# Kernel tuning notes

Hardware: AMD Instinct MI355X
Metric: run time of the kernel (lower is better)

Reference implementation:

```python
import jax, jax.numpy as jnp
import numpy as np

K = 1024  # codebook size
D = 256   # embedding dim


def setup_inputs() -> dict:
    key = jax.random.key(0)
    k1, k2 = jax.random.split(key)
    z_e_x = jax.random.normal(k1, (32, D, 32, 32), dtype=jnp.float32)  # NCHW
    # nn.Embedding weight initialized uniform(-1/K, 1/K)
    W = jax.random.uniform(k2, (K, D), dtype=jnp.float32, minval=-1.0 / K, maxval=1.0 / K)
    return {"z_e_x": z_e_x, "W": W}


def reference(z_e_x, W):
    # permute NCHW -> NHWC, flatten spatial, nearest-codebook lookup (vq)
    z = jnp.transpose(z_e_x, (0, 2, 3, 1))            # [B, H, Wd, D]
    B, H, Wd, Dd = z.shape
    flat = z.reshape(-1, Dd)                           # [N, D]
    # squared L2 distances: ||z||^2 - 2 z.W^T + ||W||^2
    z_sq = jnp.sum(flat * flat, axis=1, keepdims=True)         # [N, 1]
    w_sq = jnp.sum(W * W, axis=1)                               # [K]
    dists = z_sq - 2.0 * (flat @ W.T) + w_sq[None, :]           # [N, K]
    idx = jnp.argmin(dists, axis=1)                             # [N]
    latents = idx.reshape(B, H, Wd)                             # [B, H, Wd] int indices
    return latents
```

## Files before the change

kernel.cpp:

```cpp
#include <hip/hip_runtime.h>

#define NPOS 32768
#define DDIM 256
#define KCODES 1024

typedef __attribute__((ext_vector_type(8))) short bf16x8;
typedef __attribute__((ext_vector_type(4))) float f32x4;
typedef unsigned long long u64;

__device__ __forceinline__ float sqr_rn(float x) {
    float r = x * x;
    asm volatile("" : "+v"(r));
    return r;
}
__device__ __forceinline__ float add_rn(float a, float b) {
    float r = a + b;
    asm volatile("" : "+v"(r));
    return r;
}

__device__ __forceinline__ unsigned short f2bf(float x) {
    unsigned u = __float_as_uint(x);
    return (unsigned short)((u + 0x7fffu + ((u >> 16) & 1u)) >> 16);
}

__device__ __forceinline__ u64 packm(float s, int code) {
    unsigned b = __float_as_uint(s);
    unsigned mm = ((unsigned)((int)b >> 31)) | 0x80000000u;
    return ((u64)(b ^ mm) << 32) | (unsigned)code;
}

__device__ __forceinline__ void gld16(const void* g, void* lds) {
    __builtin_amdgcn_global_load_lds(
        (const __attribute__((address_space(1))) unsigned int*)g,
        (__attribute__((address_space(3))) unsigned int*)lds, 16, 0, 0);
}

__global__ __launch_bounds__(256) void zconv(const float* __restrict__ z,
                                             unsigned short* __restrict__ zb16t) {
    __shared__ unsigned short Ls[8 * 1024];
    const int t   = threadIdx.x;
    const int img = blockIdx.x >> 5;
    const int dc  = blockIdx.x & 31;
    const int kk  = dc >> 2, kq = dc & 3;
    const float* zr = z + img * (DDIM * 1024) + dc * 8 * 1024;
#pragma unroll
    for (int e = 0; e < 8; ++e) {
        const float4 v = *(const float4*)&zr[e * 1024 + t * 4];
        unsigned short* o = &Ls[e * 1024 + t * 4];
        o[0] = f2bf(v.x); o[1] = f2bf(v.y); o[2] = f2bf(v.z); o[3] = f2bf(v.w);
    }
    __syncthreads();
#pragma unroll
    for (int j = 0; j < 4; ++j) {
        const int m = t + j * 256;
        const int mtile = img * 8 + (m >> 7);
        bf16x8 o;
#pragma unroll
        for (int e = 0; e < 8; ++e) o[e] = (short)Ls[e * 1024 + m];
        *(bf16x8*)&zb16t[mtile * 32768 + kk * 4096 + kq * 1024 + (m & 127) * 8] = o;
    }
}

__global__ __launch_bounds__(256) void wprep(const float* __restrict__ W,
                                             float* __restrict__ wsq,
                                             unsigned short* __restrict__ wb16t) {
    const int t   = threadIdx.x;
    const int row = blockIdx.x * 16 + (t >> 4);
    const int j   = t & 15;
    const float* base = W + row * DDIM + (j & 7) + (j >> 3) * 128;
    float r = sqr_rn(base[0]);
#pragma unroll
    for (int i = 1; i < 16; ++i) r = add_rn(r, sqr_rn(base[i * 8]));
#pragma unroll
    for (int m = 1; m <= 8; m <<= 1) r = add_rn(r, __shfl_xor(r, m));
    if (j == 0) wsq[row] = r;

#pragma unroll
    for (int jj = 0; jj < 2; ++jj) {
        const int u  = t + jj * 256;
        const int n  = blockIdx.x * 16 + (u >> 5);
        const int k8 = u & 31;
        const float4 f0 = *(const float4*)&W[n * DDIM + k8 * 8];
        const float4 f1 = *(const float4*)&W[n * DDIM + k8 * 8 + 4];
        bf16x8 o;
        o[0] = (short)f2bf(f0.x); o[1] = (short)f2bf(f0.y);
        o[2] = (short)f2bf(f0.z); o[3] = (short)f2bf(f0.w);
        o[4] = (short)f2bf(f1.x); o[5] = (short)f2bf(f1.y);
        o[6] = (short)f2bf(f1.z); o[7] = (short)f2bf(f1.w);
        const int kk = k8 >> 2, kq = k8 & 3;
        *(bf16x8*)&wb16t[(n >> 8) * 65536 + kk * 8192 + kq * 2048 + (n & 255) * 8] = o;
    }
}

__global__ __launch_bounds__(256) __attribute__((amdgpu_waves_per_eu(2, 2)))
void gemm_top2(const unsigned short* __restrict__ zb16t,
               const unsigned short* __restrict__ wb16t,
               const float* __restrict__ wsq, u64* __restrict__ cand) {
    __shared__ u64 redU[4096];
    char* Ab = (char*)redU;
    char* Bb = (char*)redU + 8192;

    const int t    = threadIdx.x;
    const int w    = t >> 6;
    const int l    = t & 63;
    const int lg   = l * 16;
    const int ln   = l & 15;
    const int q    = l >> 4;
    const int mw   = (w & 1) * 64;
    const int nw   = (w >> 1) * 128;
    const int mblk = blockIdx.x >> 2;
    const int nblk = blockIdx.x & 3;
    const int m0   = mblk * 128;
    const int n0   = nblk * 256;

    const char* Az = (const char*)zb16t + (size_t)mblk * 65536;
    const char* Bz = (const char*)wb16t + (size_t)nblk * 131072;

    f32x4 acc[4][8];
#pragma unroll
    for (int a = 0; a < 4; ++a)
#pragma unroll
        for (int b = 0; b < 8; ++b) acc[a][b] = (f32x4)(0.f);

#pragma unroll 1
    for (int kk = 0; kk < 8; ++kk) {
        const char* a = Az + kk * 8192 + lg;
        const char* b = Bz + kk * 16384 + lg;
        gld16(a + w * 1024,        Ab + w * 1024);
        gld16(a + (4 + w) * 1024,  Ab + (4 + w) * 1024);
        gld16(b + w * 1024,        Bb + w * 1024);
        gld16(b + (4 + w) * 1024,  Bb + (4 + w) * 1024);
        gld16(b + (8 + w) * 1024,  Bb + (8 + w) * 1024);
        gld16(b + (12 + w) * 1024, Bb + (12 + w) * 1024);
        __syncthreads();
        bf16x8 afr[4];
#pragma unroll
        for (int mf = 0; mf < 4; ++mf)
            afr[mf] = *(const bf16x8*)(Ab + q * 2048 + (mw + mf * 16 + ln) * 16);
#pragma unroll
        for (int nf = 0; nf < 8; ++nf) {
            const bf16x8 bfr = *(const bf16x8*)(Bb + q * 4096 + (nw + nf * 16 + ln) * 16);
#pragma unroll
            for (int mf = 0; mf < 4; ++mf)
                acc[mf][nf] = __builtin_amdgcn_mfma_f32_16x16x32_bf16(
                    afr[mf], bfr, acc[mf][nf], 0, 0, 0);
        }
        __syncthreads();
    }

    float wq[8];
#pragma unroll
    for (int nf = 0; nf < 8; ++nf) wq[nf] = wsq[n0 + nw + nf * 16 + ln];

#pragma unroll
    for (int mf = 0; mf < 4; ++mf) {
#pragma unroll
        for (int reg = 0; reg < 4; ++reg) {
            const int row = mw + mf * 16 + q * 4 + reg;
            float s0 = 1e30f, s1 = 1e30f;
            int   i0 = 0,     i1 = 0;
#pragma unroll
            for (int nf = 0; nf < 8; ++nf) {
                const float s  = fmaf(-2.f, acc[mf][nf][reg], wq[nf]);
                const int   cc = n0 + nw + nf * 16 + ln;
                if (s < s0)      { s1 = s0; i1 = i0; s0 = s; i0 = cc; }
                else if (s < s1) { s1 = s; i1 = cc; }
            }
            u64 p0 = packm(s0, i0), p1 = packm(s1, i1);
            const u64 o0 = __shfl_xor(p0, 1);
            const u64 o1 = __shfl_xor(p1, 1);
            const u64 c0 = (p0 < o0) ? p0 : o0;
            const u64 hi = (p0 < o0) ? o0 : p0;
            const u64 lo = (p1 < o1) ? p1 : o1;
            const u64 c1 = (hi < lo) ? hi : lo;
            if ((ln & 1) == 0) {
                u64* slot = &redU[row * 32 + (w >> 1) * 16 + (ln >> 1) * 2];
                slot[0] = c0;
                slot[1] = c1;
            }
        }
    }
    __syncthreads();
    {
        const int r2 = t >> 1, half = t & 1;
        u64 c0 = ~0ull, c1 = ~0ull;
#pragma unroll
        for (int j = 0; j < 16; ++j) {
            const u64 v = redU[r2 * 32 + half * 16 + j];
            if (v < c0)      { c1 = c0; c0 = v; }
            else if (v < c1) { c1 = v; }
        }
        __syncthreads();
        redU[r2 * 4 + half * 2]     = c0;
        redU[r2 * 4 + half * 2 + 1] = c1;
    }
    __syncthreads();
    if (t < 128) {
        const u64 a = redU[t * 4], b = redU[t * 4 + 1];
        const u64 c = redU[t * 4 + 2], d = redU[t * 4 + 3];
        const u64 m1 = (a < c) ? a : c;
        const u64 hi = (a < c) ? c : a;
        const u64 lo = (b < d) ? b : d;
        const u64 m2 = (hi < lo) ? hi : lo;
        u64* o = &cand[(u64)(m0 + t) * 8 + nblk * 2];
        o[0] = m1;
        o[1] = m2;
    }
}

#define ZS 260
__global__ __launch_bounds__(256) void rescore(const float* __restrict__ z,
                                               const float* __restrict__ W,
                                               const float* __restrict__ wsq,
                                               const u64* __restrict__ cand,
                                               int* __restrict__ out) {
    __shared__ float Zs[32 * ZS];
    const int t  = threadIdx.x;
    const int m0 = blockIdx.x * 32;
    const float* zimg = z + (m0 >> 10) * (DDIM * 1024) + (m0 & 1023);
#pragma unroll
    for (int j = 0; j < 8; ++j) {
        const int f4 = t + j * 256;
        const int d = f4 >> 3, p4 = f4 & 7;
        const float4 v = *(const float4*)&zimg[d * 1024 + p4 * 4];
        Zs[(p4 * 4 + 0) * ZS + d] = v.x;
        Zs[(p4 * 4 + 1) * ZS + d] = v.y;
        Zs[(p4 * 4 + 2) * ZS + d] = v.z;
        Zs[(p4 * 4 + 3) * ZS + d] = v.w;
    }
    __syncthreads();
    const int pl = t >> 3, slot = t & 7;
    const int p = m0 + pl;
    const float* zr = &Zs[pl * ZS];

    float h0 = sqr_rn(zr[slot]);
    float h1 = sqr_rn(zr[128 + slot]);
#pragma unroll
    for (int i = 1; i < 16; ++i) {
        h0 = add_rn(h0, sqr_rn(zr[slot + 8 * i]));
        h1 = add_rn(h1, sqr_rn(zr[128 + slot + 8 * i]));
    }
#pragma unroll
    for (int m = 1; m <= 4; m <<= 1) {
        h0 = add_rn(h0, __shfl_xor(h0, m));
        h1 = add_rn(h1, __shfl_xor(h1, m));
    }
    const float zq = add_rn(h0, h1);

    const int code = (int)(unsigned)(cand[(u64)p * 8 + slot] & 0xffffffffULL);
    const float* wr = W + code * DDIM;
    float M = 0.f;
#pragma unroll 8
    for (int d4 = 0; d4 < 64; ++d4) {
        const float4 zv = *(const float4*)&zr[d4 * 4];
        const float4 wv = *(const float4*)&wr[d4 * 4];
        M = fmaf(zv.x, wv.x, M);
        M = fmaf(zv.y, wv.y, M);
        M = fmaf(zv.z, wv.z, M);
        M = fmaf(zv.w, wv.w, M);
    }
    const float s = add_rn(fmaf(-2.f, M, zq), wsq[code]);
    u64 v = ((u64)__float_as_uint(s) << 32) | (unsigned)code;
#pragma unroll
    for (int m = 1; m <= 4; m <<= 1) {
        const u64 o = __shfl_xor(v, m);
        if (o < v) v = o;
    }
    if (slot == 0) out[p] = (int)(unsigned)(v & 0xffffffffULL);
}

extern "C" void kernel_launch(void* const* d_in, const int* in_sizes, int n_in,
                              void* d_out, int out_size, void* d_ws, size_t ws_size,
                              hipStream_t stream) {
    const float* z = (const float*)d_in[0];
    const float* W = (const float*)d_in[1];
    int* out = (int*)d_out;

    char* ws = (char*)d_ws;
    float*          wsq   = (float*)ws;
    u64*            cand  = (u64*)(ws + 4096);
    unsigned short* zb16t = (unsigned short*)(ws + 2101248);
    unsigned short* wb16t = (unsigned short*)(ws + 18878464);

    wprep<<<KCODES / 16, 256, 0, stream>>>(W, wsq, wb16t);
    zconv<<<32 * 32, 256, 0, stream>>>(z, zb16t);
    gemm_top2<<<(NPOS / 128) * 4, 256, 0, stream>>>(zb16t, wb16t, wsq, cand);
    rescore<<<NPOS / 32, 256, 0, stream>>>(z, W, wsq, cand, out);
}
```

Baseline: 149.0 us.

## Merge prep kernels and load GEMM fragments directly from global memory

Combines the W and z conversion kernels into a single launch, using a block-index split, to save one kernel launch. The GEMM main loop stops staging A and B tiles through LDS with global_load_lds and barriers. Each lane now reads its bf16 MFMA fragments straight from the pre-swizzled global layout. This removes the LDS round trip and both syncthreads per k-step, at the cost of redundant global and L2 traffic across waves that share fragments, and less latency hiding.

```diff
diff --git a/kernel.cpp b/kernel.cpp
--- a/kernel.cpp
+++ b/kernel.cpp
@@ -30,66 +30,60 @@
     return ((u64)(b ^ mm) << 32) | (unsigned)code;
 }
 
-__device__ __forceinline__ void gld16(const void* g, void* lds) {
-    __builtin_amdgcn_global_load_lds(
-        (const __attribute__((address_space(1))) unsigned int*)g,
-        (__attribute__((address_space(3))) unsigned int*)lds, 16, 0, 0);
-}
-
-__global__ __launch_bounds__(256) void zconv(const float* __restrict__ z,
-                                             unsigned short* __restrict__ zb16t) {
+__global__ __launch_bounds__(256) void prep(const float* __restrict__ z,
+                                            const float* __restrict__ W,
+                                            float* __restrict__ wsq,
+                                            unsigned short* __restrict__ zb16t,
+                                            unsigned short* __restrict__ wb16t) {
     __shared__ unsigned short Ls[8 * 1024];
-    const int t   = threadIdx.x;
-    const int img = blockIdx.x >> 5;
-    const int dc  = blockIdx.x & 31;
-    const int kk  = dc >> 2, kq = dc & 3;
-    const float* zr = z + img * (DDIM * 1024) + dc * 8 * 1024;
-#pragma unroll
-    for (int e = 0; e < 8; ++e) {
-        const float4 v = *(const float4*)&zr[e * 1024 + t * 4];
-        unsigned short* o = &Ls[e * 1024 + t * 4];
-        o[0] = f2bf(v.x); o[1] = f2bf(v.y); o[2] = f2bf(v.z); o[3] = f2bf(v.w);
-    }
-    __syncthreads();
-#pragma unroll
-    for (int j = 0; j < 4; ++j) {
-        const int m = t + j * 256;
-        const int mtile = img * 8 + (m >> 7);
-        bf16x8 o;
-#pragma unroll
-        for (int e = 0; e < 8; ++e) o[e] = (short)Ls[e * 1024 + m];
-        *(bf16x8*)&zb16t[mtile * 32768 + kk * 4096 + kq * 1024 + (m & 127) * 8] = o;
-    }
-}
-
-__global__ __launch_bounds__(256) void wprep(const float* __restrict__ W,
-                                             float* __restrict__ wsq,
-                                             unsigned short* __restrict__ wb16t) {
-    const int t   = threadIdx.x;
-    const int row = blockIdx.x * 16 + (t >> 4);
-    const int j   = t & 15;
-    const float* base = W + row * DDIM + (j & 7) + (j >> 3) * 128;
-    float r = sqr_rn(base[0]);
-#pragma unroll
-    for (int i = 1; i < 16; ++i) r = add_rn(r, sqr_rn(base[i * 8]));
-#pragma unroll
-    for (int m = 1; m <= 8; m <<= 1) r = add_rn(r, __shfl_xor(r, m));
-    if (j == 0) wsq[row] = r;
-
-#pragma unroll
-    for (int jj = 0; jj < 2; ++jj) {
-        const int u  = t + jj * 256;
-        const int n  = blockIdx.x * 16 + (u >> 5);
-        const int k8 = u & 31;
-        const float4 f0 = *(const float4*)&W[n * DDIM + k8 * 8];
-        const float4 f1 = *(const float4*)&W[n * DDIM + k8 * 8 + 4];
-        bf16x8 o;
-        o[0] = (short)f2bf(f0.x); o[1] = (short)f2bf(f0.y);
-        o[2] = (short)f2bf(f0.z); o[3] = (short)f2bf(f0.w);
-        o[4] = (short)f2bf(f1.x); o[5] = (short)f2bf(f1.y);
-        o[6] = (short)f2bf(f1.z); o[7] = (short)f2bf(f1.w);
-        const int kk = k8 >> 2, kq = k8 & 3;
-        *(bf16x8*)&wb16t[(n >> 8) * 65536 + kk * 8192 + kq * 2048 + (n & 255) * 8] = o;
+    const int t = threadIdx.x;
+    if (blockIdx.x < 1024) {
+        const int img = blockIdx.x >> 5;
+        const int dc  = blockIdx.x & 31;
+        const int kk  = dc >> 2, kq = dc & 3;
+        const float* zr = z + img * (DDIM * 1024) + dc * 8 * 1024;
+#pragma unroll
+        for (int e = 0; e < 8; ++e) {
+            const float4 v = *(const float4*)&zr[e * 1024 + t * 4];
+            unsigned short* o = &Ls[e * 1024 + t * 4];
+            o[0] = f2bf(v.x); o[1] = f2bf(v.y); o[2] = f2bf(v.z); o[3] = f2bf(v.w);
+        }
+        __syncthreads();
+#pragma unroll
+        for (int j = 0; j < 4; ++j) {
+            const int m = t + j * 256;
+            const int mtile = img * 8 + (m >> 7);
+            bf16x8 o;
+#pragma unroll
+            for (int e = 0; e < 8; ++e) o[e] = (short)Ls[e * 1024 + m];
+            *(bf16x8*)&zb16t[mtile * 32768 + kk * 4096 + kq * 1024 + (m & 127) * 8] = o;
+        }
+    } else {
+        const int bid = blockIdx.x - 1024;
+        const int row = bid * 16 + (t >> 4);
+        const int j   = t & 15;
+        const float* base = W + row * DDIM + (j & 7) + (j >> 3) * 128;
+        float r = sqr_rn(base[0]);
+#pragma unroll
+        for (int i = 1; i < 16; ++i) r = add_rn(r, sqr_rn(base[i * 8]));
+#pragma unroll
+        for (int m = 1; m <= 8; m <<= 1) r = add_rn(r, __shfl_xor(r, m));
+        if (j == 0) wsq[row] = r;
+#pragma unroll
+        for (int jj = 0; jj < 2; ++jj) {
+            const int u  = t + jj * 256;
+            const int n  = bid * 16 + (u >> 5);
+            const int k8 = u & 31;
+            const float4 f0 = *(const float4*)&W[n * DDIM + k8 * 8];
+            const float4 f1 = *(const float4*)&W[n * DDIM + k8 * 8 + 4];
+            bf16x8 o;
+            o[0] = (short)f2bf(f0.x); o[1] = (short)f2bf(f0.y);
+            o[2] = (short)f2bf(f0.z); o[3] = (short)f2bf(f0.w);
+            o[4] = (short)f2bf(f1.x); o[5] = (short)f2bf(f1.y);
+            o[6] = (short)f2bf(f1.z); o[7] = (short)f2bf(f1.w);
+            const int kk = k8 >> 2, kq = k8 & 3;
+            *(bf16x8*)&wb16t[(n >> 8) * 65536 + kk * 8192 + kq * 2048 + (n & 255) * 8] = o;
+        }
     }
 }
 
@@ -98,13 +92,10 @@
                const unsigned short* __restrict__ wb16t,
                const float* __restrict__ wsq, u64* __restrict__ cand) {
     __shared__ u64 redU[4096];
-    char* Ab = (char*)redU;
-    char* Bb = (char*)redU + 8192;
 
     const int t    = threadIdx.x;
     const int w    = t >> 6;
     const int l    = t & 63;
-    const int lg   = l * 16;
     const int ln   = l & 15;
     const int q    = l >> 4;
     const int mw   = (w & 1) * 64;
@@ -114,8 +105,8 @@
     const int m0   = mblk * 128;
     const int n0   = nblk * 256;
 
-    const char* Az = (const char*)zb16t + (size_t)mblk * 65536;
-    const char* Bz = (const char*)wb16t + (size_t)nblk * 131072;
+    const char* aLane = (const char*)zb16t + (size_t)mblk * 65536 + q * 2048 + (mw + ln) * 16;
+    const char* bLane = (const char*)wb16t + (size_t)nblk * 131072 + q * 4096 + (nw + ln) * 16;
 
     f32x4 acc[4][8];
 #pragma unroll
@@ -125,28 +116,19 @@
 
 #pragma unroll 1
     for (int kk = 0; kk < 8; ++kk) {
-        const char* a = Az + kk * 8192 + lg;
-        const char* b = Bz + kk * 16384 + lg;
-        gld16(a + w * 1024,        Ab + w * 1024);
-        gld16(a + (4 + w) * 1024,  Ab + (4 + w) * 1024);
-        gld16(b + w * 1024,        Bb + w * 1024);
-        gld16(b + (4 + w) * 1024,  Bb + (4 + w) * 1024);
-        gld16(b + (8 + w) * 1024,  Bb + (8 + w) * 1024);
-        gld16(b + (12 + w) * 1024, Bb + (12 + w) * 1024);
-        __syncthreads();
-        bf16x8 afr[4];
+        bf16x8 afr[4], bfr[8];
 #pragma unroll
         for (int mf = 0; mf < 4; ++mf)
-            afr[mf] = *(const bf16x8*)(Ab + q * 2048 + (mw + mf * 16 + ln) * 16);
-#pragma unroll
-        for (int nf = 0; nf < 8; ++nf) {
-            const bf16x8 bfr = *(const bf16x8*)(Bb + q * 4096 + (nw + nf * 16 + ln) * 16);
+            afr[mf] = *(const bf16x8*)(aLane + kk * 8192 + mf * 256);
+#pragma unroll
+        for (int nf = 0; nf < 8; ++nf)
+            bfr[nf] = *(const bf16x8*)(bLane + kk * 16384 + nf * 256);
+#pragma unroll
+        for (int nf = 0; nf < 8; ++nf)
 #pragma unroll
             for (int mf = 0; mf < 4; ++mf)
                 acc[mf][nf] = __builtin_amdgcn_mfma_f32_16x16x32_bf16(
-                    afr[mf], bfr, acc[mf][nf], 0, 0, 0);
-        }
-        __syncthreads();
+                    afr[mf], bfr[nf], acc[mf][nf], 0, 0, 0);
     }
 
     float wq[8];
@@ -283,8 +265,7 @@
     unsigned short* zb16t = (unsigned short*)(ws + 2101248);
     unsigned short* wb16t = (unsigned short*)(ws + 18878464);
 
-    wprep<<<KCODES / 16, 256, 0, stream>>>(W, wsq, wb16t);
-    zconv<<<32 * 32, 256, 0, stream>>>(z, zb16t);
+    prep<<<1024 + KCODES / 16, 256, 0, stream>>>(z, W, wsq, zb16t, wb16t);
     gemm_top2<<<(NPOS / 128) * 4, 256, 0, stream>>>(zb16t, wb16t, wsq, cand);
     rescore<<<NPOS / 32, 256, 0, stream>>>(z, W, wsq, cand, out);
 }
```

Result: slower. 153.3 us (+2.9%).
